# Optimization experiments

Hardware: AMD Instinct MI355X
Metric: run time of the kernel (lower is better)

Reference implementation:

```python
import jax, jax.numpy as jnp
import numpy as np


def setup_inputs() -> dict:
    key = jax.random.key(0)
    k1, k2 = jax.random.split(key)
    inputs = jax.random.normal(k1, (4, 128, 64, 64), dtype=jnp.float32)
    # binary hole mask (1 = known background, 0 = hole), broadcast over channels
    mask = jnp.round(jax.random.uniform(k2, (4, 1, 64, 64), dtype=jnp.float32))
    return {"inputs": inputs, "mask": mask}


def reference(inputs, mask):
    # SFFA contextual attention with 1x1 dynamic kernels.
    # Note: in the original torch code the 1x1 conv with padding=1 produces
    # border scores that conv_transpose2d with padding=1 crops away exactly,
    # so the math reduces to per-pixel matmul + softmax + matmul.
    bz, nc, h, w = inputs.shape
    N = h * w
    background = inputs * mask                              # [b, c, h, w]
    # dynamic kernels: one nc-dim vector per background pixel (patch)
    K = background.reshape(bz, nc, N).transpose(0, 2, 1) + 1e-7   # [b, N, c]
    Kn = K / jnp.sqrt(jnp.sum(K * K, axis=2, keepdims=True))      # l2-normalized
    feat = inputs.reshape(bz, nc, N)                        # [b, c, N]
    scores = jnp.einsum('bpc,bcn->bpn', Kn, feat)           # [b, N(patch), N(pixel)]
    attn = jax.nn.softmax(scores, axis=1)                   # softmax over patches p
    agg = jnp.einsum('bpc,bpn->bcn', K, attn).reshape(bz, nc, h, w)
    return background + agg * (1.0 - mask)
```

## Files before the change

### kernel.cpp

```cpp
#include <hip/hip_runtime.h>
#include <hip/hip_bf16.h>

typedef __attribute__((ext_vector_type(8))) short bf16x8;
typedef __attribute__((ext_vector_type(4))) float f32x4;

#define NPIX 4096
#define NC   128
#define RS128 0.08838834764831845f

__global__ __launch_bounds__(1024) void sffa_prep(
    const float* __restrict__ x, const float* __restrict__ mask,
    ushort* __restrict__ KnW, ushort* __restrict__ QW, ushort* __restrict__ VtW,
    float* __restrict__ s0c, int* __restrict__ pixQ, int* __restrict__ cnts,
    float* __restrict__ out)
{
    __shared__ float xs[128][69];
    __shared__ float ms[64];
    __shared__ float rinv[64];
    __shared__ float ssum[64];
    __shared__ float2 part[16][64];
    __shared__ int se[64];
    __shared__ int bgn[64];
    __shared__ int tinfo[2];
    __shared__ int wredP[16], wredT[16];
    const int tid = threadIdx.x;
    const int b = blockIdx.x >> 6, nblk = blockIdx.x & 63;
    const int n0 = nblk * 64;
    const float* xb = x + (size_t)b * NC * NPIX;
    float* ob = out + (size_t)b * NC * NPIX;

    #pragma unroll
    for (int it = 0; it < 2; ++it) {
        int e4 = it * 1024 + tid;
        int c = e4 >> 4, n4 = (e4 & 15) * 4;
        float4 v = *(const float4*)(xb + (size_t)c * NPIX + n0 + n4);
        xs[c][n4+0] = v.x; xs[c][n4+1] = v.y; xs[c][n4+2] = v.z; xs[c][n4+3] = v.w;
        *(float4*)(ob + (size_t)c * NPIX + n0 + n4) = v;
    }
    if (tid < 16) {
        float4 mv = *(const float4*)(mask + (size_t)b * NPIX + n0 + tid * 4);
        ms[tid*4+0] = mv.x; ms[tid*4+1] = mv.y; ms[tid*4+2] = mv.z; ms[tid*4+3] = mv.w;
    }
    {
        const int lane = tid & 63, w = tid >> 6;
        float4 mv = *(const float4*)(mask + (size_t)b * NPIX + tid * 4);
        int f0 = mv.x < 0.5f ? 0x10000 : 1;
        int f1 = mv.y < 0.5f ? 0x10000 : 1;
        int f2 = mv.z < 0.5f ? 0x10000 : 1;
        int f3 = mv.w < 0.5f ? 0x10000 : 1;
        int p0 = tid * 4;
        int pre = 0, tot = f0 + f1 + f2 + f3;
        if (p0 + 0 < n0) pre += f0;
        if (p0 + 1 < n0) pre += f1;
        if (p0 + 2 < n0) pre += f2;
        if (p0 + 3 < n0) pre += f3;
        #pragma unroll
        for (int d = 1; d < 64; d <<= 1) {
            pre += __shfl_xor(pre, d);
            tot += __shfl_xor(tot, d);
        }
        if (lane == 0) { wredP[w] = pre; wredT[w] = tot; }
    }
    __syncthreads();
    if (tid < 64) {
        int vP = (tid < 16) ? wredP[tid] : 0;
        int vT = (tid < 16) ? wredT[tid] : 0;
        #pragma unroll
        for (int d = 1; d < 16; d <<= 1) {
            vP += __shfl_xor(vP, d);
            vT += __shfl_xor(vT, d);
        }
        int base  = __shfl(vP, 0);
        int total = __shfl(vT, 0);
        if (tid == 0 && nblk == 0) {
            cnts[b * 2]     = total & 0xffff;
            cnts[b * 2 + 1] = total >> 16;
        }
        int f = ms[tid] > 0.5f ? 1 : 0x10000;
        int s = f;
        #pragma unroll
        for (int d = 1; d < 64; d <<= 1) {
            int t = __shfl_up(s, d);
            if (tid >= d) s += t;
        }
        se[tid] = base + s - f;
    }
    __syncthreads();
    {
        int p = tid & 63, qd = tid >> 6;
        float m = ms[p];
        float s2 = 0.f, s1 = 0.f;
        #pragma unroll
        for (int i = 0; i < 8; ++i) {
            float xv = xs[qd*8 + i][p];
            float k = fmaf(xv, m, 1e-7f);
            s2 = fmaf(k, k, s2);
            s1 += xv;
        }
        part[qd][p] = make_float2(s2, s1);
    }
    __syncthreads();
    if (tid < 64) {
        float s2 = 0.f, s1 = 0.f;
        #pragma unroll
        for (int k = 0; k < 16; ++k) { float2 t = part[k][tid]; s2 += t.x; s1 += t.y; }
        rinv[tid] = rsqrtf(s2);
        ssum[tid] = s1 * RS128;
    }
    __syncthreads();
    #pragma unroll
    for (int it = 0; it < 4; ++it) {
        int e2 = it * 1024 + tid;
        int n = e2 >> 6, cp = (e2 & 63) * 2;
        int pe = se[n];
        float x0 = xs[cp][n], x1 = xs[cp+1][n];
        if (ms[n] > 0.5f) {
            int slot = pe & 0xffff;
            float k0 = x0 + 1e-7f, k1 = x1 + 1e-7f;
            float r = rinv[n];
            __hip_bfloat162 kn;
            kn.x = __float2bfloat16(k0 * r); kn.y = __float2bfloat16(k1 * r);
            *(__hip_bfloat162*)(KnW + ((size_t)b * NPIX + slot) * NC + cp) = kn;
        } else {
            int slot = pe >> 16;
            __hip_bfloat162 q;
            q.x = __float2bfloat16(x0); q.y = __float2bfloat16(x1);
            *(__hip_bfloat162*)(QW + ((size_t)b * NPIX + slot) * NC + cp) = q;
        }
    }
    if (tid < 64) {
        if (ms[tid] < 0.5f) {
            int slot = se[tid] >> 16;
            s0c [(size_t)b * NPIX + slot] = ssum[tid];
            pixQ[(size_t)b * NPIX + slot] = n0 + tid;
        } else {
            bgn[(se[tid] & 0xffff) - (se[0] & 0xffff)] = tid;
        }
    }
    if (tid == 0) {
        tinfo[0] = se[0] & 0xffff;
        tinfo[1] = (se[63] & 0xffff) + (ms[63] > 0.5f ? 1 : 0) - (se[0] & 0xffff);
    }
    __syncthreads();
    {
        const int s0b = tinfo[0], nbg = tinfo[1];
        const int j = tid & 63, cg = tid >> 6;
        if (j < nbg) {
            int n = bgn[j];
            ushort* vcol = VtW + (size_t)b * NC * NPIX + s0b + j;
            #pragma unroll
            for (int cc = 0; cc < 8; ++cc) {
                int c = cg * 8 + cc;
                __hip_bfloat16 h = __float2bfloat16(xs[c][n] + 1e-7f);
                vcol[(size_t)c * NPIX] = *(ushort*)&h;
            }
        }
    }
}

#define L_BUF 32768
#define L_P   65536
#define L_ML  75776
#define L_SZ  76800

__global__ __launch_bounds__(512, 4) void sffa_attn(
    const ushort* __restrict__ KnW, const ushort* __restrict__ QW,
    const ushort* __restrict__ VtW, const int* __restrict__ cnts,
    ushort* __restrict__ partW, float* __restrict__ mlW, int KS)
{
    __shared__ __align__(16) char smem[L_SZ];
    const int tid  = threadIdx.x;
    const int w = tid >> 6, lane = tid & 63;
    const int l15 = lane & 15, g = lane >> 4;
    const int bx = (int)blockIdx.x;
    const int per = 64 * KS;
    const int b = bx / per;
    const int rem = bx - b * per;
    const int qblk = rem / KS, ks = rem - (rem / KS) * KS;
    const int q0 = qblk * 64;
    const int cntK = cnts[b * 2], cntQ = cnts[b * 2 + 1];
    if (q0 >= cntQ) return;
    const int blk = (b * 64 + qblk) * KS + ks;

    const int nk64 = (cntK + 63) >> 6;
    const int tpk  = (nk64 + KS - 1) / KS;
    const int t0   = ks * tpk;
    const int t1   = min(t0 + tpk, nk64);
    const int NTK  = t1 - t0;

    if (NTK <= 0) {
        unsigned* pz = (unsigned*)(partW + (size_t)blk * 8192);
        #pragma unroll
        for (int i = 0; i < 8; ++i) pz[i * 512 + tid] = 0u;
        if (tid < 64)
            *(float2*)(mlW + ((size_t)blk * 64 + tid) * 2) = make_float2(-1e30f, 0.f);
        return;
    }

    const int half = w >> 2;
    const int wq   = w & 3;
    const int kbase = t0 * 64;

    const ushort* Knb = KnW + (size_t)b * NPIX * NC;
    const ushort* Qb  = QW  + (size_t)b * NPIX * NC + (size_t)q0 * NC;
    const ushort* Vtb = VtW + (size_t)b * NC * NPIX;

    #pragma unroll
    for (int it = 0; it < 2; ++it) {
        int L = (it * 512 + tid) * 16;
        int row = L >> 8, col = L & 255;
        int4 v = *(const int4*)((const char*)Qb + L);
        *(int4*)(smem + row * 256 + (col ^ ((row & 15) << 4))) = v;
    }
    __syncthreads();
    bf16x8 qf[4];
    {
        int qrow = wq * 16 + l15;
        #pragma unroll
        for (int kc = 0; kc < 4; ++kc)
            qf[kc] = *(const bf16x8*)(smem + qrow * 256 + ((64*kc + 16*g) ^ (l15 << 4)));
    }
    __syncthreads();

    const int kOff = (tid >> 4) * 256 + (((tid & 15) * 16) ^ (((tid >> 4) & 15) << 4));
    const int cV = tid >> 3, sV = tid & 7;
    const int vOff = cV * 128 + ((sV * 16) ^ ((cV & 7) << 4));
    const int4* kgbase = (const int4*)(Knb + (size_t)kbase * NC);
    const ushort* vgbase = Vtb + (size_t)cV * NPIX + kbase + sV * 8;

    int4 pr0, pr1, pr2, pr3;
    pr0 = kgbase[tid]; pr1 = kgbase[512 + tid];
    pr2 = *(const int4*)(vgbase);
    pr3 = *(const int4*)(vgbase + (size_t)64 * NPIX);
    {
        char* base = smem;
        *(int4*)(base + kOff) = pr0;
        *(int4*)(base + kOff + 8192) = pr1;
        *(int4*)(base + 16384 + vOff) = pr2;
        *(int4*)(base + 16384 + vOff + 8192) = pr3;
    }
    if (NTK > 1) {
        pr0 = kgbase[1024 + tid]; pr1 = kgbase[1536 + tid];
        pr2 = *(const int4*)(vgbase + 64);
        pr3 = *(const int4*)(vgbase + (size_t)64 * NPIX + 64);
    }
    __syncthreads();

    f32x4 acc[8];
    const f32x4 fzero = {0.f, 0.f, 0.f, 0.f};
    #pragma unroll
    for (int i = 0; i < 8; ++i) acc[i] = fzero;
    float mrun = -1e30f, lrun = 0.f;
    char* Pw = smem + L_P + w * 1280;

    for (int kt = 0; kt < NTK; ++kt) {
        if (kt + 1 < NTK) {
            char* base = smem + ((kt + 1) & 1) * L_BUF;
            *(int4*)(base + kOff) = pr0;
            *(int4*)(base + kOff + 8192) = pr1;
            *(int4*)(base + 16384 + vOff) = pr2;
            *(int4*)(base + 16384 + vOff + 8192) = pr3;
        }
        if (kt + 2 < NTK) {
            pr0 = kgbase[(kt + 2) * 1024 + tid];
            pr1 = kgbase[(kt + 2) * 1024 + 512 + tid];
            pr2 = *(const int4*)(vgbase + (kt + 2) * 64);
            pr3 = *(const int4*)(vgbase + (size_t)64 * NPIX + (kt + 2) * 64);
        }
        char* bb = smem + (kt & 1) * L_BUF;
        f32x4 sa0 = fzero, sa1 = fzero;
        {
            const char* rb0 = bb + (half * 32 + l15) * 256;
            const char* rb1 = rb0 + 4096;
            const int sw = l15 << 4;
            __builtin_amdgcn_s_setprio(1);
            #pragma unroll
            for (int kc = 0; kc < 4; ++kc) {
                int off = (64 * kc + 16 * g) ^ sw;
                bf16x8 a0 = *(const bf16x8*)(rb0 + off);
                bf16x8 a1 = *(const bf16x8*)(rb1 + off);
                sa0 = __builtin_amdgcn_mfma_f32_16x16x32_bf16(a0, qf[kc], sa0, 0, 0, 0);
                sa1 = __builtin_amdgcn_mfma_f32_16x16x32_bf16(a1, qf[kc], sa1, 0, 0, 0);
            }
            __builtin_amdgcn_s_setprio(0);
        }
        {
            int kg0 = (t0 + kt) * 64;
            if (kg0 + 64 > cntK) {
                int kb = cntK - kg0;
                int kr = half * 32 + 4 * g;
                #pragma unroll
                for (int r = 0; r < 4; ++r) {
                    if (kr + r >= kb)      sa0[r] = -3e38f;
                    if (kr + 16 + r >= kb) sa1[r] = -3e38f;
                }
            }
        }
        float tmax = fmaxf(fmaxf(fmaxf(sa0[0], sa0[1]), fmaxf(sa0[2], sa0[3])),
                           fmaxf(fmaxf(sa1[0], sa1[1]), fmaxf(sa1[2], sa1[3])));
        tmax = fmaxf(tmax, __shfl_xor(tmax, 16));
        tmax = fmaxf(tmax, __shfl_xor(tmax, 32));
        bool grow = !__all(tmax <= mrun + 8.f);
        float mnew = grow ? fmaxf(mrun, tmax) : mrun;
        float p0[4], p1[4];
        float ts = 0.f;
        #pragma unroll
        for (int r = 0; r < 4; ++r) { p0[r] = __expf(sa0[r] - mnew); ts += p0[r]; }
        #pragma unroll
        for (int r = 0; r < 4; ++r) { p1[r] = __expf(sa1[r] - mnew); ts += p1[r]; }
        ts += __shfl_xor(ts, 16);
        ts += __shfl_xor(ts, 32);
        if (grow) {
            float sc = __expf(mrun - mnew);
            lrun = lrun * sc + ts;
            float scr[4];
            #pragma unroll
            for (int r = 0; r < 4; ++r) scr[r] = __shfl(sc, 4 * g + r);
            #pragma unroll
            for (int ct = 0; ct < 8; ++ct) {
                acc[ct][0] *= scr[0]; acc[ct][1] *= scr[1];
                acc[ct][2] *= scr[2]; acc[ct][3] *= scr[3];
            }
            mrun = mnew;
        } else {
            lrun += ts;
        }
        union { __hip_bfloat162 h; unsigned u; } ua0, ua1, ub0, ub1;
        ua0.h.x = __float2bfloat16(p0[0]); ua0.h.y = __float2bfloat16(p0[1]);
        ua1.h.x = __float2bfloat16(p0[2]); ua1.h.y = __float2bfloat16(p0[3]);
        ub0.h.x = __float2bfloat16(p1[0]); ub0.h.y = __float2bfloat16(p1[1]);
        ub1.h.x = __float2bfloat16(p1[2]); ub1.h.y = __float2bfloat16(p1[3]);
        *(int2*)(Pw + l15 * 80 +      8 * g) = make_int2((int)ua0.u, (int)ua1.u);
        *(int2*)(Pw + l15 * 80 + 32 + 8 * g) = make_int2((int)ub0.u, (int)ub1.u);
        bf16x8 pf = *(const bf16x8*)(Pw + l15 * 80 + 16 * g);
        {
            const char* vb = bb + 16384;
            __builtin_amdgcn_s_setprio(1);
            #pragma unroll
            for (int ct = 0; ct < 8; ++ct) {
                int c = 16 * ct + l15;
                bf16x8 vf = *(const bf16x8*)(vb + c * 128 +
                                             ((64 * half + 16 * g) ^ ((c & 7) << 4)));
                acc[ct] = __builtin_amdgcn_mfma_f32_16x16x32_bf16(pf, vf, acc[ct], 0, 0, 0);
            }
            __builtin_amdgcn_s_setprio(0);
        }
        __syncthreads();
    }

    float* ma = (float*)(smem + L_ML);
    float* la = ma + 64; float* mb = la + 64; float* lb = mb + 64;
    const int q = wq * 16 + l15;
    if (g == 0) {
        if (half == 0) { ma[q] = mrun; la[q] = lrun; }
        else           { mb[q] = mrun; lb[q] = lrun; }
    }
    __syncthreads();
    float* agg = (float*)smem;
    {
        float mstar = fmaxf(ma[q], mb[q]);
        float f = __expf(mrun - mstar);
        float fr[4];
        #pragma unroll
        for (int r = 0; r < 4; ++r) fr[r] = __shfl(f, 4 * g + r);
        if (half == 1) {
            #pragma unroll
            for (int ct = 0; ct < 8; ++ct) {
                int c = 16 * ct + l15;
                #pragma unroll
                for (int r = 0; r < 4; ++r)
                    agg[c * 68 + wq * 16 + 4 * g + r] = acc[ct][r] * fr[r];
            }
        }
        __syncthreads();
        if (half == 0) {
            #pragma unroll
            for (int ct = 0; ct < 8; ++ct) {
                int c = 16 * ct + l15;
                #pragma unroll
                for (int r = 0; r < 4; ++r) {
                    int idx = c * 68 + wq * 16 + 4 * g + r;
                    agg[idx] = acc[ct][r] * fr[r] + agg[idx];
                }
            }
        }
    }
    __syncthreads();
    if (tid < 64) {
        float M = fmaxf(ma[tid], mb[tid]);
        float ls = la[tid] * __expf(ma[tid] - M) + lb[tid] * __expf(mb[tid] - M);
        *(float2*)(mlW + ((size_t)blk * 64 + tid) * 2) = make_float2(M, ls);
    }
    ushort* pdst = partW + (size_t)blk * 8192;
    #pragma unroll
    for (int it = 0; it < 8; ++it) {
        int idx = it * 512 + tid;
        int c = idx >> 5, n2 = (idx & 31) * 2;
        __hip_bfloat162 h;
        h.x = __float2bfloat16(agg[c * 68 + n2]);
        h.y = __float2bfloat16(agg[c * 68 + n2 + 1]);
        *(__hip_bfloat162*)(pdst + c * 64 + n2) = h;
    }
}

__global__ __launch_bounds__(256) void sffa_comb(
    const ushort* __restrict__ partW, const float* __restrict__ mlW,
    const float* __restrict__ s0c, const int* __restrict__ pixQ,
    const int* __restrict__ cnts, float* __restrict__ out, int KS)
{
    __shared__ float wgtL[4][64];
    __shared__ int pixnL[64];
    const int tid = threadIdx.x;
    const int bx = blockIdx.x;
    const int b = bx >> 8, qb = (bx >> 2) & 63, ch = bx & 3;
    const int cntK = cnts[b * 2], cntQ = cnts[b * 2 + 1];
    if (qb * 64 >= cntQ) return;
    const int blkbase = (b * 64 + qb) * KS;
    const float m0f = (float)(NPIX - cntK);

    if (tid < 64) {
        int slot = qb * 64 + tid;
        int pix = -1;
        if (slot < cntQ) {
            pix = pixQ[(size_t)b * NPIX + slot];
            float s0 = s0c[(size_t)b * NPIX + slot];
            float M = s0;
            float2 mls[4];
            #pragma unroll
            for (int k = 0; k < 4; ++k) {
                if (k < KS) {
                    mls[k] = *(const float2*)(mlW + ((size_t)(blkbase + k) * 64 + tid) * 2);
                    M = fmaxf(M, mls[k].x);
                }
            }
            float L = m0f * __expf(s0 - M);
            #pragma unroll
            for (int k = 0; k < 4; ++k)
                if (k < KS) L += mls[k].y * __expf(mls[k].x - M);
            float Li = 1.f / L;
            #pragma unroll
            for (int k = 0; k < 4; ++k)
                if (k < KS) wgtL[k][tid] = __expf(mls[k].x - M) * Li;
        }
        pixnL[tid] = pix;
    }
    __syncthreads();

    float* ob = out + (size_t)b * NC * NPIX;
    const ushort* pb = partW + (size_t)blkbase * 8192;
    {
        int cl = tid >> 3, grp = tid & 7;
        int c = ch * 32 + cl;
        float v[8] = {0.f,0.f,0.f,0.f,0.f,0.f,0.f,0.f};
        #pragma unroll
        for (int k = 0; k < 4; ++k) {
            if (k < KS) {
                ushort u[8];
                *(int4*)u = *(const int4*)(pb + (size_t)k * 8192 + c * 64 + grp * 8);
                #pragma unroll
                for (int j = 0; j < 8; ++j)
                    v[j] = fmaf(__uint_as_float((unsigned)u[j] << 16),
                                wgtL[k][grp * 8 + j], v[j]);
            }
        }
        #pragma unroll
        for (int j = 0; j < 8; ++j) {
            int pix = pixnL[grp * 8 + j];
            if (pix >= 0) ob[(size_t)c * NPIX + pix] = v[j];
        }
    }
}

extern "C" void kernel_launch(void* const* d_in, const int* in_sizes, int n_in,
                              void* d_out, int out_size, void* d_ws, size_t ws_size,
                              hipStream_t stream) {
    const float* x    = (const float*)d_in[0];
    const float* mask = (const float*)d_in[1];
    char* ws = (char*)d_ws;
    const size_t MBy = 1024 * 1024;
    const size_t KBy = 1024;

    ushort* KnW = (ushort*)(ws);
    ushort* QW  = (ushort*)(ws + 4 * MBy);
    ushort* VtW = (ushort*)(ws + 8 * MBy);

    size_t need4 = 12 * MBy + 4 * 4 * MBy + 1 * MBy;
    int KS = (ws_size >= need4) ? 4 : 2;
    ushort* partW = (ushort*)(ws + 12 * MBy);
    char* tail = ws + 12 * MBy + (size_t)KS * 4 * MBy;
    float* mlW    = (float*)(tail);
    float* s0c    = (float*)(tail + 576 * KBy);
    int*   pixQ   = (int*)(tail + 640 * KBy);
    int*   cnts   = (int*)(tail + 704 * KBy);

    sffa_prep <<<256, 1024, 0, stream>>>(x, mask, KnW, QW, VtW, s0c, pixQ, cnts,
                                         (float*)d_out);
    sffa_attn <<<4 * 64 * KS, 512, 0, stream>>>(KnW, QW, VtW, cnts, partW, mlW, KS);
    sffa_comb <<<4 * 64 * 4, 256, 0, stream>>>(partW, mlW, s0c, pixQ, cnts,
                                               (float*)d_out, KS);
}
```

Before: 53.38 us.

## Fuse split-K combine into attention kernel via last-block atomic ticket

Removes the separate combine kernel launch. Each attention block bumps a per-query-block atomic ticket once its partial results are written, and the last block of each group merges the partials into the output. The prep kernel resets the tickets. This saves one launch and its tail latency, at the cost of fences, an atomic and a serialized combine on the last-arriving block.

```diff
diff --git a/kernel.cpp b/kernel.cpp
--- a/kernel.cpp
+++ b/kernel.cpp
@@ -12,7 +12,7 @@
     const float* __restrict__ x, const float* __restrict__ mask,
     ushort* __restrict__ KnW, ushort* __restrict__ QW, ushort* __restrict__ VtW,
     float* __restrict__ s0c, int* __restrict__ pixQ, int* __restrict__ cnts,
-    float* __restrict__ out)
+    float* __restrict__ out, int* __restrict__ tickets)
 {
     __shared__ float xs[128][69];
     __shared__ float ms[64];
@@ -28,6 +28,8 @@
     const int n0 = nblk * 64;
     const float* xb = x + (size_t)b * NC * NPIX;
     float* ob = out + (size_t)b * NC * NPIX;
+
+    if (tid == 0) tickets[blockIdx.x] = 0;
 
     #pragma unroll
     for (int it = 0; it < 2; ++it) {
@@ -166,9 +168,12 @@
 __global__ __launch_bounds__(512, 4) void sffa_attn(
     const ushort* __restrict__ KnW, const ushort* __restrict__ QW,
     const ushort* __restrict__ VtW, const int* __restrict__ cnts,
-    ushort* __restrict__ partW, float* __restrict__ mlW, int KS)
+    ushort* __restrict__ partW, float* __restrict__ mlW,
+    const float* __restrict__ s0c, const int* __restrict__ pixQ,
+    float* __restrict__ out, int* __restrict__ tickets, int KS)
 {
     __shared__ __align__(16) char smem[L_SZ];
+    __shared__ int lastFlag;
     const int tid  = threadIdx.x;
     const int w = tid >> 6, lane = tid & 63;
     const int l15 = lane & 15, g = lane >> 4;
@@ -188,238 +193,235 @@
     const int t1   = min(t0 + tpk, nk64);
     const int NTK  = t1 - t0;
 
-    if (NTK <= 0) {
-        unsigned* pz = (unsigned*)(partW + (size_t)blk * 8192);
-        #pragma unroll
-        for (int i = 0; i < 8; ++i) pz[i * 512 + tid] = 0u;
-        if (tid < 64)
-            *(float2*)(mlW + ((size_t)blk * 64 + tid) * 2) = make_float2(-1e30f, 0.f);
-        return;
-    }
-
-    const int half = w >> 2;
-    const int wq   = w & 3;
-    const int kbase = t0 * 64;
-
-    const ushort* Knb = KnW + (size_t)b * NPIX * NC;
-    const ushort* Qb  = QW  + (size_t)b * NPIX * NC + (size_t)q0 * NC;
-    const ushort* Vtb = VtW + (size_t)b * NC * NPIX;
-
-    #pragma unroll
-    for (int it = 0; it < 2; ++it) {
-        int L = (it * 512 + tid) * 16;
-        int row = L >> 8, col = L & 255;
-        int4 v = *(const int4*)((const char*)Qb + L);
-        *(int4*)(smem + row * 256 + (col ^ ((row & 15) << 4))) = v;
-    }
-    __syncthreads();
-    bf16x8 qf[4];
-    {
-        int qrow = wq * 16 + l15;
-        #pragma unroll
-        for (int kc = 0; kc < 4; ++kc)
-            qf[kc] = *(const bf16x8*)(smem + qrow * 256 + ((64*kc + 16*g) ^ (l15 << 4)));
-    }
-    __syncthreads();
-
-    const int kOff = (tid >> 4) * 256 + (((tid & 15) * 16) ^ (((tid >> 4) & 15) << 4));
-    const int cV = tid >> 3, sV = tid & 7;
-    const int vOff = cV * 128 + ((sV * 16) ^ ((cV & 7) << 4));
-    const int4* kgbase = (const int4*)(Knb + (size_t)kbase * NC);
-    const ushort* vgbase = Vtb + (size_t)cV * NPIX + kbase + sV * 8;
-
-    int4 pr0, pr1, pr2, pr3;
-    pr0 = kgbase[tid]; pr1 = kgbase[512 + tid];
-    pr2 = *(const int4*)(vgbase);
-    pr3 = *(const int4*)(vgbase + (size_t)64 * NPIX);
-    {
-        char* base = smem;
-        *(int4*)(base + kOff) = pr0;
-        *(int4*)(base + kOff + 8192) = pr1;
-        *(int4*)(base + 16384 + vOff) = pr2;
-        *(int4*)(base + 16384 + vOff + 8192) = pr3;
-    }
-    if (NTK > 1) {
-        pr0 = kgbase[1024 + tid]; pr1 = kgbase[1536 + tid];
-        pr2 = *(const int4*)(vgbase + 64);
-        pr3 = *(const int4*)(vgbase + (size_t)64 * NPIX + 64);
-    }
-    __syncthreads();
-
-    f32x4 acc[8];
-    const f32x4 fzero = {0.f, 0.f, 0.f, 0.f};
-    #pragma unroll
-    for (int i = 0; i < 8; ++i) acc[i] = fzero;
-    float mrun = -1e30f, lrun = 0.f;
-    char* Pw = smem + L_P + w * 1280;
-
-    for (int kt = 0; kt < NTK; ++kt) {
-        if (kt + 1 < NTK) {
-            char* base = smem + ((kt + 1) & 1) * L_BUF;
+    if (NTK > 0) {
+        const int half = w >> 2;
+        const int wq   = w & 3;
+        const int kbase = t0 * 64;
+
+        const ushort* Knb = KnW + (size_t)b * NPIX * NC;
+        const ushort* Qb  = QW  + (size_t)b * NPIX * NC + (size_t)q0 * NC;
+        const ushort* Vtb = VtW + (size_t)b * NC * NPIX;
+
+        #pragma unroll
+        for (int it = 0; it < 2; ++it) {
+            int L = (it * 512 + tid) * 16;
+            int row = L >> 8, col = L & 255;
+            int4 v = *(const int4*)((const char*)Qb + L);
+            *(int4*)(smem + row * 256 + (col ^ ((row & 15) << 4))) = v;
+        }
+        __syncthreads();
+        bf16x8 qf[4];
+        {
+            int qrow = wq * 16 + l15;
+            #pragma unroll
+            for (int kc = 0; kc < 4; ++kc)
+                qf[kc] = *(const bf16x8*)(smem + qrow * 256 + ((64*kc + 16*g) ^ (l15 << 4)));
+        }
+        __syncthreads();
+
+        const int kOff = (tid >> 4) * 256 + (((tid & 15) * 16) ^ (((tid >> 4) & 15) << 4));
+        const int cV = tid >> 3, sV = tid & 7;
+        const int vOff = cV * 128 + ((sV * 16) ^ ((cV & 7) << 4));
+        const int4* kgbase = (const int4*)(Knb + (size_t)kbase * NC);
+        const ushort* vgbase = Vtb + (size_t)cV * NPIX + kbase + sV * 8;
+
+        int4 pr0, pr1, pr2, pr3;
+        pr0 = kgbase[tid]; pr1 = kgbase[512 + tid];
+        pr2 = *(const int4*)(vgbase);
+        pr3 = *(const int4*)(vgbase + (size_t)64 * NPIX);
+        {
+            char* base = smem;
             *(int4*)(base + kOff) = pr0;
             *(int4*)(base + kOff + 8192) = pr1;
             *(int4*)(base + 16384 + vOff) = pr2;
             *(int4*)(base + 16384 + vOff + 8192) = pr3;
         }
-        if (kt + 2 < NTK) {
-            pr0 = kgbase[(kt + 2) * 1024 + tid];
-            pr1 = kgbase[(kt + 2) * 1024 + 512 + tid];
-            pr2 = *(const int4*)(vgbase + (kt + 2) * 64);
-            pr3 = *(const int4*)(vgbase + (size_t)64 * NPIX + (kt + 2) * 64);
-        }
-        char* bb = smem + (kt & 1) * L_BUF;
-        f32x4 sa0 = fzero, sa1 = fzero;
+        if (NTK > 1) {
+            pr0 = kgbase[1024 + tid]; pr1 = kgbase[1536 + tid];
+            pr2 = *(const int4*)(vgbase + 64);
+            pr3 = *(const int4*)(vgbase + (size_t)64 * NPIX + 64);
+        }
+        __syncthreads();
+
+        f32x4 acc[8];
+        const f32x4 fzero = {0.f, 0.f, 0.f, 0.f};
+        #pragma unroll
+        for (int i = 0; i < 8; ++i) acc[i] = fzero;
+        float mrun = -1e30f, lrun = 0.f;
+        char* Pw = smem + L_P + w * 1280;
+
+        for (int kt = 0; kt < NTK; ++kt) {
+            if (kt + 1 < NTK) {
+                char* base = smem + ((kt + 1) & 1) * L_BUF;
+                *(int4*)(base + kOff) = pr0;
+                *(int4*)(base + kOff + 8192) = pr1;
+                *(int4*)(base + 16384 + vOff) = pr2;
+                *(int4*)(base + 16384 + vOff + 8192) = pr3;
+            }
+            if (kt + 2 < NTK) {
+                pr0 = kgbase[(kt + 2) * 1024 + tid];
+                pr1 = kgbase[(kt + 2) * 1024 + 512 + tid];
+                pr2 = *(const int4*)(vgbase + (kt + 2) * 64);
+                pr3 = *(const int4*)(vgbase + (size_t)64 * NPIX + (kt + 2) * 64);
+            }
+            char* bb = smem + (kt & 1) * L_BUF;
+            f32x4 sa0 = fzero, sa1 = fzero;
+            {
+                const char* rb0 = bb + (half * 32 + l15) * 256;
+                const char* rb1 = rb0 + 4096;
+                const int sw = l15 << 4;
+                __builtin_amdgcn_s_setprio(1);
+                #pragma unroll
+                for (int kc = 0; kc < 4; ++kc) {
+                    int off = (64 * kc + 16 * g) ^ sw;
+                    bf16x8 a0 = *(const bf16x8*)(rb0 + off);
+                    bf16x8 a1 = *(const bf16x8*)(rb1 + off);
+                    sa0 = __builtin_amdgcn_mfma_f32_16x16x32_bf16(a0, qf[kc], sa0, 0, 0, 0);
+                    sa1 = __builtin_amdgcn_mfma_f32_16x16x32_bf16(a1, qf[kc], sa1, 0, 0, 0);
+                }
+                __builtin_amdgcn_s_setprio(0);
+            }
+            {
+                int kg0 = (t0 + kt) * 64;
+                if (kg0 + 64 > cntK) {
+                    int kb = cntK - kg0;
+                    int kr = half * 32 + 4 * g;
+                    #pragma unroll
+                    for (int r = 0; r < 4; ++r) {
+                        if (kr + r >= kb)      sa0[r] = -3e38f;
+                        if (kr + 16 + r >= kb) sa1[r] = -3e38f;
+                    }
+                }
+            }
+            float tmax = fmaxf(fmaxf(fmaxf(sa0[0], sa0[1]), fmaxf(sa0[2], sa0[3])),
+                               fmaxf(fmaxf(sa1[0], sa1[1]), fmaxf(sa1[2], sa1[3])));
+            tmax = fmaxf(tmax, __shfl_xor(tmax, 16));
+            tmax = fmaxf(tmax, __shfl_xor(tmax, 32));
+            bool grow = !__all(tmax <= mrun + 8.f);
+            float mnew = grow ? fmaxf(mrun, tmax) : mrun;
+            float p0[4], p1[4];
+            float ts = 0.f;
+            #pragma unroll
+            for (int r = 0; r < 4; ++r) { p0[r] = __expf(sa0[r] - mnew); ts += p0[r]; }
+            #pragma unroll
+            for (int r = 0; r < 4; ++r) { p1[r] = __expf(sa1[r] - mnew); ts += p1[r]; }
+            ts += __shfl_xor(ts, 16);
+            ts += __shfl_xor(ts, 32);
+            if (grow) {
+                float sc = __expf(mrun - mnew);
+                lrun = lrun * sc + ts;
+                float scr[4];
+                #pragma unroll
+                for (int r = 0; r < 4; ++r) scr[r] = __shfl(sc, 4 * g + r);
+                #pragma unroll
+                for (int ct = 0; ct < 8; ++ct) {
+                    acc[ct][0] *= scr[0]; acc[ct][1] *= scr[1];
+                    acc[ct][2] *= scr[2]; acc[ct][3] *= scr[3];
+                }
+                mrun = mnew;
+            } else {
+                lrun += ts;
+            }
+            union { __hip_bfloat162 h; unsigned u; } ua0, ua1, ub0, ub1;
+            ua0.h.x = __float2bfloat16(p0[0]); ua0.h.y = __float2bfloat16(p0[1]);
+            ua1.h.x = __float2bfloat16(p0[2]); ua1.h.y = __float2bfloat16(p0[3]);
+            ub0.h.x = __float2bfloat16(p1[0]); ub0.h.y = __float2bfloat16(p1[1]);
+            ub1.h.x = __float2bfloat16(p1[2]); ub1.h.y = __float2bfloat16(p1[3]);
+            *(int2*)(Pw + l15 * 80 +      8 * g) = make_int2((int)ua0.u, (int)ua1.u);
+            *(int2*)(Pw + l15 * 80 + 32 + 8 * g) = make_int2((int)ub0.u, (int)ub1.u);
+            bf16x8 pf = *(const bf16x8*)(Pw + l15 * 80 + 16 * g);
+            {
+                const char* vb = bb + 16384;
+                __builtin_amdgcn_s_setprio(1);
+                #pragma unroll
+                for (int ct = 0; ct < 8; ++ct) {
+                    int c = 16 * ct + l15;
+                    bf16x8 vf = *(const bf16x8*)(vb + c * 128 +
+                                                 ((64 * half + 16 * g) ^ ((c & 7) << 4)));
+                    acc[ct] = __builtin_amdgcn_mfma_f32_16x16x32_bf16(pf, vf, acc[ct], 0, 0, 0);
+                }
+                __builtin_amdgcn_s_setprio(0);
+            }
+            __syncthreads();
+        }
+
+        float* ma = (float*)(smem + L_ML);
+        float* la = ma + 64; float* mb = la + 64; float* lb = mb + 64;
+        const int q = wq * 16 + l15;
+        if (g == 0) {
+            if (half == 0) { ma[q] = mrun; la[q] = lrun; }
+            else           { mb[q] = mrun; lb[q] = lrun; }
+        }
+        __syncthreads();
+        float* agg = (float*)smem;
         {
-            const char* rb0 = bb + (half * 32 + l15) * 256;
-            const char* rb1 = rb0 + 4096;
-            const int sw = l15 << 4;
-            __builtin_amdgcn_s_setprio(1);
-            #pragma unroll
-            for (int kc = 0; kc < 4; ++kc) {
-                int off = (64 * kc + 16 * g) ^ sw;
-                bf16x8 a0 = *(const bf16x8*)(rb0 + off);
-                bf16x8 a1 = *(const bf16x8*)(rb1 + off);
-                sa0 = __builtin_amdgcn_mfma_f32_16x16x32_bf16(a0, qf[kc], sa0, 0, 0, 0);
-                sa1 = __builtin_amdgcn_mfma_f32_16x16x32_bf16(a1, qf[kc], sa1, 0, 0, 0);
-            }
-            __builtin_amdgcn_s_setprio(0);
-        }
-        {
-            int kg0 = (t0 + kt) * 64;
-            if (kg0 + 64 > cntK) {
-                int kb = cntK - kg0;
-                int kr = half * 32 + 4 * g;
-                #pragma unroll
-                for (int r = 0; r < 4; ++r) {
-                    if (kr + r >= kb)      sa0[r] = -3e38f;
-                    if (kr + 16 + r >= kb) sa1[r] = -3e38f;
-                }
-            }
-        }
-        float tmax = fmaxf(fmaxf(fmaxf(sa0[0], sa0[1]), fmaxf(sa0[2], sa0[3])),
-                           fmaxf(fmaxf(sa1[0], sa1[1]), fmaxf(sa1[2], sa1[3])));
-        tmax = fmaxf(tmax, __shfl_xor(tmax, 16));
-        tmax = fmaxf(tmax, __shfl_xor(tmax, 32));
-        bool grow = !__all(tmax <= mrun + 8.f);
-        float mnew = grow ? fmaxf(mrun, tmax) : mrun;
-        float p0[4], p1[4];
-        float ts = 0.f;
-        #pragma unroll
-        for (int r = 0; r < 4; ++r) { p0[r] = __expf(sa0[r] - mnew); ts += p0[r]; }
-        #pragma unroll
-        for (int r = 0; r < 4; ++r) { p1[r] = __expf(sa1[r] - mnew); ts += p1[r]; }
-        ts += __shfl_xor(ts, 16);
-        ts += __shfl_xor(ts, 32);
-        if (grow) {
-            float sc = __expf(mrun - mnew);
-            lrun = lrun * sc + ts;
-            float scr[4];
-            #pragma unroll
-            for (int r = 0; r < 4; ++r) scr[r] = __shfl(sc, 4 * g + r);
-            #pragma unroll
-            for (int ct = 0; ct < 8; ++ct) {
-                acc[ct][0] *= scr[0]; acc[ct][1] *= scr[1];
-                acc[ct][2] *= scr[2]; acc[ct][3] *= scr[3];
-            }
-            mrun = mnew;
-        } else {
-            lrun += ts;
-        }
-        union { __hip_bfloat162 h; unsigned u; } ua0, ua1, ub0, ub1;
-        ua0.h.x = __float2bfloat16(p0[0]); ua0.h.y = __float2bfloat16(p0[1]);
-        ua1.h.x = __float2bfloat16(p0[2]); ua1.h.y = __float2bfloat16(p0[3]);
-        ub0.h.x = __float2bfloat16(p1[0]); ub0.h.y = __float2bfloat16(p1[1]);
-        ub1.h.x = __float2bfloat16(p1[2]); ub1.h.y = __float2bfloat16(p1[3]);
-        *(int2*)(Pw + l15 * 80 +      8 * g) = make_int2((int)ua0.u, (int)ua1.u);
-        *(int2*)(Pw + l15 * 80 + 32 + 8 * g) = make_int2((int)ub0.u, (int)ub1.u);
-        bf16x8 pf = *(const bf16x8*)(Pw + l15 * 80 + 16 * g);
-        {
-            const char* vb = bb + 16384;
-            __builtin_amdgcn_s_setprio(1);
-            #pragma unroll
-            for (int ct = 0; ct < 8; ++ct) {
-                int c = 16 * ct + l15;
-                bf16x8 vf = *(const bf16x8*)(vb + c * 128 +
-                                             ((64 * half + 16 * g) ^ ((c & 7) << 4)));
-                acc[ct] = __builtin_amdgcn_mfma_f32_16x16x32_bf16(pf, vf, acc[ct], 0, 0, 0);
-            }
-            __builtin_amdgcn_s_setprio(0);
+            float mstar = fmaxf(ma[q], mb[q]);
+            float f = __expf(mrun - mstar);
+            float fr[4];
+            #pragma unroll
+            for (int r = 0; r < 4; ++r) fr[r] = __shfl(f, 4 * g + r);
+            if (half == 1) {
+                #pragma unroll
+                for (int ct = 0; ct < 8; ++ct) {
+                    int c = 16 * ct + l15;
+                    #pragma unroll
+                    for (int r = 0; r < 4; ++r)
+                        agg[c * 68 + wq * 16 + 4 * g + r] = acc[ct][r] * fr[r];
+                }
+            }
+            __syncthreads();
+            if (half == 0) {
+                #pragma unroll
+                for (int ct = 0; ct < 8; ++ct) {
+                    int c = 16 * ct + l15;
+                    #pragma unroll
+                    for (int r = 0; r < 4; ++r) {
+                        int idx = c * 68 + wq * 16 + 4 * g + r;
+                        agg[idx] = acc[ct][r] * fr[r] + agg[idx];
+                    }
+                }
+            }
         }
         __syncthreads();
-    }
-
-    float* ma = (float*)(smem + L_ML);
-    float* la = ma + 64; float* mb = la + 64; float* lb = mb + 64;
-    const int q = wq * 16 + l15;
-    if (g == 0) {
-        if (half == 0) { ma[q] = mrun; la[q] = lrun; }
-        else           { mb[q] = mrun; lb[q] = lrun; }
-    }
-    __syncthreads();
-    float* agg = (float*)smem;
-    {
-        float mstar = fmaxf(ma[q], mb[q]);
-        float f = __expf(mrun - mstar);
-        float fr[4];
-        #pragma unroll
-        for (int r = 0; r < 4; ++r) fr[r] = __shfl(f, 4 * g + r);
-        if (half == 1) {
-            #pragma unroll
-            for (int ct = 0; ct < 8; ++ct) {
-                int c = 16 * ct + l15;
-                #pragma unroll
-                for (int r = 0; r < 4; ++r)
-                    agg[c * 68 + wq * 16 + 4 * g + r] = acc[ct][r] * fr[r];
-            }
-        }
-        __syncthreads();
-        if (half == 0) {
-            #pragma unroll
-            for (int ct = 0; ct < 8; ++ct) {
-                int c = 16 * ct + l15;
-                #pragma unroll
-                for (int r = 0; r < 4; ++r) {
-                    int idx = c * 68 + wq * 16 + 4 * g + r;
-                    agg[idx] = acc[ct][r] * fr[r] + agg[idx];
-                }
-            }
-        }
-    }
-    __syncthreads();
+        if (tid < 64) {
+            float M = fmaxf(ma[tid], mb[tid]);
+            float ls = la[tid] * __expf(ma[tid] - M) + lb[tid] * __expf(mb[tid] - M);
+            *(float2*)(mlW + ((size_t)blk * 64 + tid) * 2) = make_float2(M, ls);
+        }
+        ushort* pdst = partW + (size_t)blk * 8192;
+        #pragma unroll
+        for (int it = 0; it < 8; ++it) {
+            int idx = it * 512 + tid;
+            int c = idx >> 5, n2 = (idx & 31) * 2;
+            __hip_bfloat162 h;
+            h.x = __float2bfloat16(agg[c * 68 + n2]);
+            h.y = __float2bfloat16(agg[c * 68 + n2 + 1]);
+            *(__hip_bfloat162*)(pdst + c * 64 + n2) = h;
+        }
+    } else {
+        unsigned* pz = (unsigned*)(partW + (size_t)blk * 8192);
+        #pragma unroll
+        for (int i = 0; i < 8; ++i) pz[i * 512 + tid] = 0u;
+        if (tid < 64)
+            *(float2*)(mlW + ((size_t)blk * 64 + tid) * 2) = make_float2(-1e30f, 0.f);
+    }
+
+    __threadfence();
+    if (tid == 0) {
+        int old = __hip_atomic_fetch_add(&tickets[b * 64 + qblk], 1,
+                                         __ATOMIC_ACQ_REL, __HIP_MEMORY_SCOPE_AGENT);
+        lastFlag = (old == KS - 1);
+    }
+    __syncthreads();
+    if (!lastFlag) return;
+    __threadfence();
+
+    const int blkbase = (b * 64 + qblk) * KS;
+    float* wgtC = (float*)smem;
+    int*   pixC = (int*)(smem + 1024);
+    const float m0f = (float)(NPIX - cntK);
     if (tid < 64) {
-        float M = fmaxf(ma[tid], mb[tid]);
-        float ls = la[tid] * __expf(ma[tid] - M) + lb[tid] * __expf(mb[tid] - M);
-        *(float2*)(mlW + ((size_t)blk * 64 + tid) * 2) = make_float2(M, ls);
-    }
-    ushort* pdst = partW + (size_t)blk * 8192;
-    #pragma unroll
-    for (int it = 0; it < 8; ++it) {
-        int idx = it * 512 + tid;
-        int c = idx >> 5, n2 = (idx & 31) * 2;
-        __hip_bfloat162 h;
-        h.x = __float2bfloat16(agg[c * 68 + n2]);
-        h.y = __float2bfloat16(agg[c * 68 + n2 + 1]);
-        *(__hip_bfloat162*)(pdst + c * 64 + n2) = h;
-    }
-}
-
-__global__ __launch_bounds__(256) void sffa_comb(
-    const ushort* __restrict__ partW, const float* __restrict__ mlW,
-    const float* __restrict__ s0c, const int* __restrict__ pixQ,
-    const int* __restrict__ cnts, float* __restrict__ out, int KS)
-{
-    __shared__ float wgtL[4][64];
-    __shared__ int pixnL[64];
-    const int tid = threadIdx.x;
-    const int bx = blockIdx.x;
-    const int b = bx >> 8, qb = (bx >> 2) & 63, ch = bx & 3;
-    const int cntK = cnts[b * 2], cntQ = cnts[b * 2 + 1];
-    if (qb * 64 >= cntQ) return;
-    const int blkbase = (b * 64 + qb) * KS;
-    const float m0f = (float)(NPIX - cntK);
-
-    if (tid < 64) {
-        int slot = qb * 64 + tid;
+        int slot = q0 + tid;
         int pix = -1;
         if (slot < cntQ) {
             pix = pixQ[(size_t)b * NPIX + slot];
@@ -440,17 +442,18 @@
             float Li = 1.f / L;
             #pragma unroll
             for (int k = 0; k < 4; ++k)
-                if (k < KS) wgtL[k][tid] = __expf(mls[k].x - M) * Li;
-        }
-        pixnL[tid] = pix;
+                if (k < KS) wgtC[k * 64 + tid] = __expf(mls[k].x - M) * Li;
+        }
+        pixC[tid] = pix;
     }
     __syncthreads();
 
     float* ob = out + (size_t)b * NC * NPIX;
     const ushort* pb = partW + (size_t)blkbase * 8192;
-    {
-        int cl = tid >> 3, grp = tid & 7;
-        int c = ch * 32 + cl;
+    #pragma unroll
+    for (int it = 0; it < 2; ++it) {
+        int idx = it * 512 + tid;
+        int c = idx >> 3, grp = idx & 7;
         float v[8] = {0.f,0.f,0.f,0.f,0.f,0.f,0.f,0.f};
         #pragma unroll
         for (int k = 0; k < 4; ++k) {
@@ -460,12 +463,12 @@
                 #pragma unroll
                 for (int j = 0; j < 8; ++j)
                     v[j] = fmaf(__uint_as_float((unsigned)u[j] << 16),
-                                wgtL[k][grp * 8 + j], v[j]);
+                                wgtC[k * 64 + grp * 8 + j], v[j]);
             }
         }
         #pragma unroll
         for (int j = 0; j < 8; ++j) {
-            int pix = pixnL[grp * 8 + j];
+            int pix = pixC[grp * 8 + j];
             if (pix >= 0) ob[(size_t)c * NPIX + pix] = v[j];
         }
     }
@@ -492,10 +495,10 @@
     float* s0c    = (float*)(tail + 576 * KBy);
     int*   pixQ   = (int*)(tail + 640 * KBy);
     int*   cnts   = (int*)(tail + 704 * KBy);
+    int*   tkts   = (int*)(tail + 708 * KBy);
 
     sffa_prep <<<256, 1024, 0, stream>>>(x, mask, KnW, QW, VtW, s0c, pixQ, cnts,
-                                         (float*)d_out);
-    sffa_attn <<<4 * 64 * KS, 512, 0, stream>>>(KnW, QW, VtW, cnts, partW, mlW, KS);
-    sffa_comb <<<4 * 64 * 4, 256, 0, stream>>>(partW, mlW, s0c, pixQ, cnts,
-                                               (float*)d_out, KS);
+                                         (float*)d_out, tkts);
+    sffa_attn <<<4 * 64 * KS, 512, 0, stream>>>(KnW, QW, VtW, cnts, partW, mlW,
+                                                s0c, pixQ, (float*)d_out, tkts, KS);
 }
```

Measured after the change: 207.6 us. +288.9%, slower.

## Drop split-K attention and fuse the combine step into the attention kernel

Applied to the files above, without the earlier changes.

Removes the key-dimension split (KS partial blocks) and the separate combine kernel. Each attention block now walks all key tiles, then does the final softmax normalisation, including the masked-patch constant term, and writes the output directly. This removes the bf16 partial-sum round trip through global memory and one kernel launch. The cost is less parallelism: only 256 blocks (at most 4 batches × 64 query blocks) each run the full key loop, which may leave most CUs of the MI355X idle.

```diff
diff --git a/kernel.cpp b/kernel.cpp
--- a/kernel.cpp
+++ b/kernel.cpp
@@ -161,45 +161,42 @@
 #define L_BUF 32768
 #define L_P   65536
 #define L_ML  75776
-#define L_SZ  76800
-
-__global__ __launch_bounds__(512, 4) void sffa_attn(
+#define L_SCL 76800
+#define L_PIX 77056
+#define L_SZ  77312
+
+__global__ __launch_bounds__(512, 2) void sffa_attn(
     const ushort* __restrict__ KnW, const ushort* __restrict__ QW,
     const ushort* __restrict__ VtW, const int* __restrict__ cnts,
-    ushort* __restrict__ partW, float* __restrict__ mlW, int KS)
+    const float* __restrict__ s0c, const int* __restrict__ pixQ,
+    float* __restrict__ out)
 {
     __shared__ __align__(16) char smem[L_SZ];
     const int tid  = threadIdx.x;
     const int w = tid >> 6, lane = tid & 63;
     const int l15 = lane & 15, g = lane >> 4;
     const int bx = (int)blockIdx.x;
-    const int per = 64 * KS;
-    const int b = bx / per;
-    const int rem = bx - b * per;
-    const int qblk = rem / KS, ks = rem - (rem / KS) * KS;
+    const int b = bx >> 6, qblk = bx & 63;
     const int q0 = qblk * 64;
     const int cntK = cnts[b * 2], cntQ = cnts[b * 2 + 1];
     if (q0 >= cntQ) return;
-    const int blk = (b * 64 + qblk) * KS + ks;
-
-    const int nk64 = (cntK + 63) >> 6;
-    const int tpk  = (nk64 + KS - 1) / KS;
-    const int t0   = ks * tpk;
-    const int t1   = min(t0 + tpk, nk64);
-    const int NTK  = t1 - t0;
+
+    const int NTK = (cntK + 63) >> 6;
+    float* ob = out + (size_t)b * NC * NPIX;
 
     if (NTK <= 0) {
-        unsigned* pz = (unsigned*)(partW + (size_t)blk * 8192);
-        #pragma unroll
-        for (int i = 0; i < 8; ++i) pz[i * 512 + tid] = 0u;
-        if (tid < 64)
-            *(float2*)(mlW + ((size_t)blk * 64 + tid) * 2) = make_float2(-1e30f, 0.f);
+        if (tid < 64) {
+            int slot = q0 + tid;
+            if (slot < cntQ) {
+                int pix = pixQ[(size_t)b * NPIX + slot];
+                for (int c = 0; c < NC; ++c) ob[(size_t)c * NPIX + pix] = 0.f;
+            }
+        }
         return;
     }
 
     const int half = w >> 2;
     const int wq   = w & 3;
-    const int kbase = t0 * 64;
 
     const ushort* Knb = KnW + (size_t)b * NPIX * NC;
     const ushort* Qb  = QW  + (size_t)b * NPIX * NC + (size_t)q0 * NC;
@@ -225,8 +222,8 @@
     const int kOff = (tid >> 4) * 256 + (((tid & 15) * 16) ^ (((tid >> 4) & 15) << 4));
     const int cV = tid >> 3, sV = tid & 7;
     const int vOff = cV * 128 + ((sV * 16) ^ ((cV & 7) << 4));
-    const int4* kgbase = (const int4*)(Knb + (size_t)kbase * NC);
-    const ushort* vgbase = Vtb + (size_t)cV * NPIX + kbase + sV * 8;
+    const int4* kgbase = (const int4*)Knb;
+    const ushort* vgbase = Vtb + (size_t)cV * NPIX + sV * 8;
 
     int4 pr0, pr1, pr2, pr3;
     pr0 = kgbase[tid]; pr1 = kgbase[512 + tid];
@@ -285,7 +282,7 @@
             __builtin_amdgcn_s_setprio(0);
         }
         {
-            int kg0 = (t0 + kt) * 64;
+            int kg0 = kt * 64;
             if (kg0 + 64 > cntK) {
                 int kb = cntK - kg0;
                 int kr = half * 32 + 4 * g;
@@ -386,87 +383,38 @@
         }
     }
     __syncthreads();
+
+    float* scl  = (float*)(smem + L_SCL);
+    int*   pixS = (int*)(smem + L_PIX);
+    const float m0f = (float)(NPIX - cntK);
     if (tid < 64) {
-        float M = fmaxf(ma[tid], mb[tid]);
-        float ls = la[tid] * __expf(ma[tid] - M) + lb[tid] * __expf(mb[tid] - M);
-        *(float2*)(mlW + ((size_t)blk * 64 + tid) * 2) = make_float2(M, ls);
-    }
-    ushort* pdst = partW + (size_t)blk * 8192;
-    #pragma unroll
-    for (int it = 0; it < 8; ++it) {
-        int idx = it * 512 + tid;
-        int c = idx >> 5, n2 = (idx & 31) * 2;
-        __hip_bfloat162 h;
-        h.x = __float2bfloat16(agg[c * 68 + n2]);
-        h.y = __float2bfloat16(agg[c * 68 + n2 + 1]);
-        *(__hip_bfloat162*)(pdst + c * 64 + n2) = h;
-    }
-}
-
-__global__ __launch_bounds__(256) void sffa_comb(
-    const ushort* __restrict__ partW, const float* __restrict__ mlW,
-    const float* __restrict__ s0c, const int* __restrict__ pixQ,
-    const int* __restrict__ cnts, float* __restrict__ out, int KS)
-{
-    __shared__ float wgtL[4][64];
-    __shared__ int pixnL[64];
-    const int tid = threadIdx.x;
-    const int bx = blockIdx.x;
-    const int b = bx >> 8, qb = (bx >> 2) & 63, ch = bx & 3;
-    const int cntK = cnts[b * 2], cntQ = cnts[b * 2 + 1];
-    if (qb * 64 >= cntQ) return;
-    const int blkbase = (b * 64 + qb) * KS;
-    const float m0f = (float)(NPIX - cntK);
-
-    if (tid < 64) {
-        int slot = qb * 64 + tid;
+        int slot = q0 + tid;
         int pix = -1;
+        float sv = 0.f;
         if (slot < cntQ) {
             pix = pixQ[(size_t)b * NPIX + slot];
+            float M  = fmaxf(ma[tid], mb[tid]);
+            float ls = la[tid] * __expf(ma[tid] - M) + lb[tid] * __expf(mb[tid] - M);
             float s0 = s0c[(size_t)b * NPIX + slot];
-            float M = s0;
-            float2 mls[4];
-            #pragma unroll
-            for (int k = 0; k < 4; ++k) {
-                if (k < KS) {
-                    mls[k] = *(const float2*)(mlW + ((size_t)(blkbase + k) * 64 + tid) * 2);
-                    M = fmaxf(M, mls[k].x);
-                }
-            }
-            float L = m0f * __expf(s0 - M);
-            #pragma unroll
-            for (int k = 0; k < 4; ++k)
-                if (k < KS) L += mls[k].y * __expf(mls[k].x - M);
-            float Li = 1.f / L;
-            #pragma unroll
-            for (int k = 0; k < 4; ++k)
-                if (k < KS) wgtL[k][tid] = __expf(mls[k].x - M) * Li;
-        }
-        pixnL[tid] = pix;
-    }
-    __syncthreads();
-
-    float* ob = out + (size_t)b * NC * NPIX;
-    const ushort* pb = partW + (size_t)blkbase * 8192;
-    {
-        int cl = tid >> 3, grp = tid & 7;
-        int c = ch * 32 + cl;
-        float v[8] = {0.f,0.f,0.f,0.f,0.f,0.f,0.f,0.f};
-        #pragma unroll
-        for (int k = 0; k < 4; ++k) {
-            if (k < KS) {
-                ushort u[8];
-                *(int4*)u = *(const int4*)(pb + (size_t)k * 8192 + c * 64 + grp * 8);
-                #pragma unroll
-                for (int j = 0; j < 8; ++j)
-                    v[j] = fmaf(__uint_as_float((unsigned)u[j] << 16),
-                                wgtL[k][grp * 8 + j], v[j]);
-            }
-        }
+            float M2 = fmaxf(M, s0);
+            float eM = __expf(M - M2);
+            float L  = m0f * __expf(s0 - M2) + ls * eM;
+            sv = eM / L;
+        }
+        scl[tid]  = sv;
+        pixS[tid] = pix;
+    }
+    __syncthreads();
+    #pragma unroll
+    for (int it = 0; it < 2; ++it) {
+        int idx = it * 512 + tid;
+        int c = idx >> 3, grp = idx & 7;
         #pragma unroll
         for (int j = 0; j < 8; ++j) {
-            int pix = pixnL[grp * 8 + j];
-            if (pix >= 0) ob[(size_t)c * NPIX + pix] = v[j];
+            int sq = grp * 8 + j;
+            int pix = pixS[sq];
+            if (pix >= 0)
+                ob[(size_t)c * NPIX + pix] = agg[c * 68 + sq] * scl[sq];
         }
     }
 }
@@ -483,19 +431,13 @@
     ushort* KnW = (ushort*)(ws);
     ushort* QW  = (ushort*)(ws + 4 * MBy);
     ushort* VtW = (ushort*)(ws + 8 * MBy);
-
-    size_t need4 = 12 * MBy + 4 * 4 * MBy + 1 * MBy;
-    int KS = (ws_size >= need4) ? 4 : 2;
-    ushort* partW = (ushort*)(ws + 12 * MBy);
-    char* tail = ws + 12 * MBy + (size_t)KS * 4 * MBy;
-    float* mlW    = (float*)(tail);
-    float* s0c    = (float*)(tail + 576 * KBy);
-    int*   pixQ   = (int*)(tail + 640 * KBy);
-    int*   cnts   = (int*)(tail + 704 * KBy);
+    char* tail = ws + 12 * MBy;
+    float* s0c  = (float*)(tail);
+    int*   pixQ = (int*)(tail + 64 * KBy);
+    int*   cnts = (int*)(tail + 128 * KBy);
 
     sffa_prep <<<256, 1024, 0, stream>>>(x, mask, KnW, QW, VtW, s0c, pixQ, cnts,
                                          (float*)d_out);
-    sffa_attn <<<4 * 64 * KS, 512, 0, stream>>>(KnW, QW, VtW, cnts, partW, mlW, KS);
-    sffa_comb <<<4 * 64 * 4, 256, 0, stream>>>(partW, mlW, s0c, pixQ, cnts,
-                                               (float*)d_out, KS);
+    sffa_attn <<<256, 512, 0, stream>>>(KnW, QW, VtW, cnts, s0c, pixQ,
+                                        (float*)d_out);
 }
```

Measured after the change: 56.84 us. +6.5%, slower.
